# Performance work log

Measured on AMD Instinct MI355X. Metric: run time of the kernel, lower is better.

The kernel has to match this reference:

```python
import jax, jax.numpy as jnp
import numpy as np

N = 100000      # nodes
E = 1600000     # edges (avg degree 16)
DIN = 128
DH = 128
DOUT = 64
K = 2           # SGConv propagation steps
EPS = 1e-5      # BatchNorm eps


def setup_inputs() -> dict:
    key = jax.random.key(0)
    ks = jax.random.split(key, 12)
    x = jax.random.normal(ks[0], (N, DIN), dtype=jnp.float32)
    edge_index = jax.random.randint(ks[1], (2, E), 0, N, dtype=jnp.int32)
    def lin(k, fin, fout):
        k1, k2 = jax.random.split(k)
        s = 1.0 / np.sqrt(fin)
        W = jax.random.uniform(k1, (fin, fout), jnp.float32, -s, s)
        b = jax.random.uniform(k2, (fout,), jnp.float32, -s, s)
        return W, b
    W1, b1 = lin(ks[2], DIN, DH)
    W2, b2 = lin(ks[3], DH, DH)
    W3, b3 = lin(ks[4], DH, DOUT)
    g1 = jnp.ones((DH,), jnp.float32); be1 = jnp.zeros((DH,), jnp.float32)
    g2 = jnp.ones((DH,), jnp.float32); be2 = jnp.zeros((DH,), jnp.float32)
    return {"x": x, "edge_index": edge_index,
            "W1": W1, "b1": b1, "g1": g1, "be1": be1,
            "W2": W2, "b2": b2, "g2": g2, "be2": be2,
            "W3": W3, "b3": b3}


def _sgc_propagate(h, row, col, norm):
    # h: [N, d]; gather source nodes, scale per-edge, scatter-add to dest
    for _ in range(K):
        msg = norm[:, None] * h[row]                      # [E, d]
        h = jax.ops.segment_sum(msg, col, num_segments=N)  # [N, d]
    return h


def _batchnorm(h, gamma, beta):
    # training-mode BN over node axis, biased variance (torch semantics)
    mu = jnp.mean(h, axis=0)
    var = jnp.mean(jnp.square(h - mu), axis=0)
    return gamma * (h - mu) * jax.lax.rsqrt(var + EPS) + beta


def reference(x, edge_index, W1, b1, g1, be1, W2, b2, g2, be2, W3, b3):
    row, col = edge_index[0], edge_index[1]
    # symmetric degree normalization; degree counted on row (as in source)
    deg = jax.ops.segment_sum(jnp.ones((E,), x.dtype), row, num_segments=N)
    dis = jnp.where(deg > 0, 1.0 / jnp.sqrt(jnp.maximum(deg, 1.0)), 0.0)
    norm = dis[row] * dis[col]                             # [E]

    h = _sgc_propagate(x, row, col, norm)
    h = _batchnorm(h @ W1 + b1, g1, be1)   # dropout p=0.0 -> identity
    h = _sgc_propagate(h, row, col, norm)
    h = _batchnorm(h @ W2 + b2, g2, be2)
    return h @ W3 + b3                      # [N, DOUT]
```

## Files before the change

kernel.cpp:

```cpp
#include <hip/hip_runtime.h>
#include <hip/hip_fp16.h>


typedef _Float16 f16x8 __attribute__((ext_vector_type(8)));
typedef __attribute__((ext_vector_type(4))) float f32x4;

#define HR_RBITS 15
#define HR_RSIZE 32768
#define HR_NRANGE 4
#define HR_NCHUNK 96
#define HR_WPC (HR_NRANGE * HR_RSIZE / 2)

#define PA_NCHUNK 256
#define PB_SHIFT 8

static inline size_t align256(size_t x) { return (x + 255) & ~(size_t)255; }

__device__ inline unsigned int packh2(float a, float b) {
    return (unsigned int)__half_as_ushort(__float2half(a)) |
           ((unsigned int)__half_as_ushort(__float2half(b)) << 16);
}

__device__ inline void fmamix_lo(float& acc, unsigned int u, float w) {
    asm("v_fma_mix_f32 %0, %1, %2, %0 op_sel_hi:[1,0,0]"
        : "+v"(acc) : "v"(u), "v"(w));
}
__device__ inline void fmamix_hi(float& acc, unsigned int u, float w) {
    asm("v_fma_mix_f32 %0, %1, %2, %0 op_sel:[1,0,0] op_sel_hi:[1,0,0]"
        : "+v"(acc) : "v"(u), "v"(w));
}

__global__ void hist_row_kernel(const int* __restrict__ row, int E,
                                unsigned int* __restrict__ staging) {
    __shared__ unsigned int l32[HR_RSIZE / 2];
    int range = blockIdx.x % HR_NRANGE;
    int chunk = blockIdx.x / HR_NRANGE;
    for (int i = threadIdx.x; i < HR_RSIZE / 2; i += 256) l32[i] = 0;
    __syncthreads();
    int lo = range << HR_RBITS;
    int q4 = E >> 2;
    int ebeg = (int)(((long long)q4 * chunk / HR_NCHUNK) << 2);
    int eend = (int)(((long long)q4 * (chunk + 1) / HR_NCHUNK) << 2);
    for (int i = ebeg + threadIdx.x * 4; i + 3 < eend; i += 256 * 4) {
        int4 v = *(const int4*)(row + i);
        unsigned a;
        a = (unsigned)(v.x - lo); if (a < HR_RSIZE) atomicAdd(&l32[a >> 1], (a & 1) ? 0x10000u : 1u);
        a = (unsigned)(v.y - lo); if (a < HR_RSIZE) atomicAdd(&l32[a >> 1], (a & 1) ? 0x10000u : 1u);
        a = (unsigned)(v.z - lo); if (a < HR_RSIZE) atomicAdd(&l32[a >> 1], (a & 1) ? 0x10000u : 1u);
        a = (unsigned)(v.w - lo); if (a < HR_RSIZE) atomicAdd(&l32[a >> 1], (a & 1) ? 0x10000u : 1u);
    }
    if (chunk == HR_NCHUNK - 1) {
        for (int i = (E & ~3) + threadIdx.x; i < E; i += 256) {
            unsigned a = (unsigned)(row[i] - lo);
            if (a < HR_RSIZE) atomicAdd(&l32[a >> 1], (a & 1) ? 0x10000u : 1u);
        }
    }
    __syncthreads();
    unsigned int* dst = staging + (size_t)chunk * HR_WPC + (lo >> 1);
    for (int i = threadIdx.x; i < HR_RSIZE / 2; i += 256) dst[i] = l32[i];
}

__global__ void dis_kernel(const unsigned int* __restrict__ staging, float* __restrict__ dis, int n) {
    int i = blockIdx.x * blockDim.x + threadIdx.x;
    if (i < n) {
        int shift = (i & 1) * 16;
        int d = 0;
#pragma unroll 4
        for (int c = 0; c < HR_NCHUNK; ++c)
            d += (staging[(size_t)c * HR_WPC + (i >> 1)] >> shift) & 0xffff;
        dis[i] = d > 0 ? rsqrtf((float)d) : 0.f;
    }
}


__global__ void pa_hist_kernel(const int* __restrict__ col, int E,
                               int* __restrict__ chunkhist, int nbuck) {
    __shared__ int lh[512];
    int chunk = blockIdx.x;
    for (int i = threadIdx.x; i < nbuck; i += 256) lh[i] = 0;
    __syncthreads();
    int ebeg = (int)((long long)E * chunk / PA_NCHUNK);
    int eend = (int)((long long)E * (chunk + 1) / PA_NCHUNK);
    for (int i = ebeg + threadIdx.x; i < eend; i += 256)
        atomicAdd(&lh[col[i] >> PB_SHIFT], 1);
    __syncthreads();
    for (int i = threadIdx.x; i < nbuck; i += 256)
        chunkhist[i * PA_NCHUNK + chunk] = lh[i];
}

__global__ void pa_scan1_kernel(int* __restrict__ chunkhist, int* __restrict__ tot) {
    __shared__ int sh[PA_NCHUNK];
    int b = blockIdx.x, t = threadIdx.x;
    int* p = chunkhist + b * PA_NCHUNK;
    int v = p[t];
    sh[t] = v;
    __syncthreads();
    for (int off = 1; off < PA_NCHUNK; off <<= 1) {
        int tv = (t >= off) ? sh[t - off] : 0;
        __syncthreads();
        sh[t] += tv;
        __syncthreads();
    }
    p[t] = sh[t] - v;
    if (t == PA_NCHUNK - 1) tot[b] = sh[t];
}

__global__ void pa_scan2_kernel(const int* __restrict__ tot, int* __restrict__ bucketstart,
                                int nbuck) {
    __shared__ int sh[512];
    int t = threadIdx.x;
    int v = (t < nbuck) ? tot[t] : 0;
    sh[t] = v;
    __syncthreads();
    for (int off = 1; off < 512; off <<= 1) {
        int tv = (t >= off) ? sh[t - off] : 0;
        __syncthreads();
        sh[t] += tv;
        __syncthreads();
    }
    if (t < nbuck) bucketstart[t] = sh[t] - v;
    if (t == 511) bucketstart[nbuck] = sh[511];
}

__global__ void pa_scatter_kernel(const int* __restrict__ row, const int* __restrict__ col,
                                  int E, const int* __restrict__ chunkhist,
                                  const int* __restrict__ bucketstart,
                                  int2* __restrict__ part, int nbuck) {
    __shared__ int loff[512];
    int chunk = blockIdx.x;
    for (int i = threadIdx.x; i < nbuck; i += 256)
        loff[i] = chunkhist[i * PA_NCHUNK + chunk] + bucketstart[i];
    __syncthreads();
    int ebeg = (int)((long long)E * chunk / PA_NCHUNK);
    int eend = (int)((long long)E * (chunk + 1) / PA_NCHUNK);
    for (int i = ebeg + threadIdx.x; i < eend; i += 256) {
        int r = row[i], c = col[i];
        int pos = atomicAdd(&loff[c >> PB_SHIFT], 1);
        int2 v; v.x = r; v.y = c;
        part[pos] = v;
    }
}

__global__ void pb_kernel(const int2* __restrict__ part, const int* __restrict__ bucketstart,
                          const float* __restrict__ dis, int2* __restrict__ csr,
                          int* __restrict__ csr_ptr, int n) {
    __shared__ int lcnt[256], sh[256], loff[256];
    int b = blockIdx.x, t = threadIdx.x;
    int nlo = b << PB_SHIFT;
    int ebeg = bucketstart[b], eend = bucketstart[b + 1];
    lcnt[t] = 0;
    __syncthreads();
    for (int i = ebeg + t; i < eend; i += 256)
        atomicAdd(&lcnt[part[i].y - nlo], 1);
    __syncthreads();
    int v = lcnt[t];
    sh[t] = v;
    __syncthreads();
    for (int off = 1; off < 256; off <<= 1) {
        int tv = (t >= off) ? sh[t - off] : 0;
        __syncthreads();
        sh[t] += tv;
        __syncthreads();
    }
    int excl = sh[t] - v;
    loff[t] = excl;
    if (nlo + t <= n) csr_ptr[nlo + t] = ebeg + excl;
    __syncthreads();
    for (int i = ebeg + t; i < eend; i += 256) {
        int2 e = part[i];
        int c = e.y;
        int slot = atomicAdd(&loff[c - nlo], 1);
        int2 o;
        o.x = e.x;
        o.y = __float_as_int(dis[e.x] * dis[c]);
        csr[ebeg + slot] = o;
    }
}


__global__ void xcvt_kernel(const float* __restrict__ x, unsigned int* __restrict__ x16, int total4) {
    for (int i = blockIdx.x * blockDim.x + threadIdx.x; i < total4; i += gridDim.x * blockDim.x) {
        float4 f = ((const float4*)x)[i];
        x16[i * 2] = packh2(f.x, f.y);
        x16[i * 2 + 1] = packh2(f.z, f.w);
    }
}

__global__ void wcvt_kernel(const float* __restrict__ W1, const float* __restrict__ W2,
                            unsigned short* __restrict__ W1t, unsigned short* __restrict__ W2t) {
    int i = blockIdx.x * blockDim.x + threadIdx.x;
    if (i < 32768) {
        const float* W = (i < 16384) ? W1 : W2;
        unsigned short* T = (i < 16384) ? W1t : W2t;
        int j = i & 16383;
        int k = j >> 7, c = j & 127;
        T[c * 128 + k] = __half_as_ushort(__float2half(W[j]));
    }
}


template <bool AFF>
__global__ void spmm16_kernel(const int* __restrict__ csr_ptr, const int2* __restrict__ csr,
                              const unsigned short* __restrict__ h_in,
                              const float* __restrict__ scale, const float* __restrict__ shift,
                              unsigned short* __restrict__ h_out, int n) {
    int gw = __builtin_amdgcn_readfirstlane((blockIdx.x * blockDim.x + threadIdx.x) >> 6);
    int lane = threadIdx.x & 63;
    int sub = lane & 15;
    int grp = lane >> 4;
    if (gw >= n) return;
    uint4* outp = (uint4*)(h_out + (size_t)gw * 128) + sub;
    int beg = csr_ptr[gw];
    int end = csr_ptr[gw + 1];
    int cnt = end - beg;
    if (cnt == 0) {
        if (lane < 16) {
            uint4 z = {0u, 0u, 0u, 0u};
            *outp = z;
        }
        return;
    }
    const int2* base = csr + beg;
    const unsigned short* hb = h_in + sub * 8;
    float acc[8];
#pragma unroll
    for (int j = 0; j < 8; ++j) acc[j] = 0.f;
    float wsum = 0.f;
    for (int j0 = 0; j0 < cnt; j0 += 16) {
        int2 ent[4];
#pragma unroll
        for (int k = 0; k < 4; ++k) ent[k] = base[j0 + 4 * k + grp];
        uint4 u[4];
        float w[4];
#pragma unroll
        for (int k = 0; k < 4; ++k) {
            bool v = (j0 + 4 * k + grp) < cnt;
            int idx = v ? ent[k].x : 0;
            w[k] = v ? __int_as_float(ent[k].y) : 0.f;
            u[k] = *(const uint4*)(hb + (size_t)((unsigned)idx * 128u));
        }
#pragma unroll
        for (int k = 0; k < 4; ++k) {
            if (AFF) wsum += w[k];
            fmamix_lo(acc[0], u[k].x, w[k]);
            fmamix_hi(acc[1], u[k].x, w[k]);
            fmamix_lo(acc[2], u[k].y, w[k]);
            fmamix_hi(acc[3], u[k].y, w[k]);
            fmamix_lo(acc[4], u[k].z, w[k]);
            fmamix_hi(acc[5], u[k].z, w[k]);
            fmamix_lo(acc[6], u[k].w, w[k]);
            fmamix_hi(acc[7], u[k].w, w[k]);
        }
    }
#pragma unroll
    for (int j = 0; j < 8; ++j) {
        acc[j] += __shfl_xor(acc[j], 16, 64);
        acc[j] += __shfl_xor(acc[j], 32, 64);
    }
    if (AFF) {
        wsum += __shfl_xor(wsum, 16, 64);
        wsum += __shfl_xor(wsum, 32, 64);
        float4 s0 = ((const float4*)scale)[sub * 2];
        float4 s1 = ((const float4*)scale)[sub * 2 + 1];
        float4 h0 = ((const float4*)shift)[sub * 2];
        float4 h1 = ((const float4*)shift)[sub * 2 + 1];
        acc[0] = fmaf(h0.x, wsum, s0.x * acc[0]);
        acc[1] = fmaf(h0.y, wsum, s0.y * acc[1]);
        acc[2] = fmaf(h0.z, wsum, s0.z * acc[2]);
        acc[3] = fmaf(h0.w, wsum, s0.w * acc[3]);
        acc[4] = fmaf(h1.x, wsum, s1.x * acc[4]);
        acc[5] = fmaf(h1.y, wsum, s1.y * acc[5]);
        acc[6] = fmaf(h1.z, wsum, s1.z * acc[6]);
        acc[7] = fmaf(h1.w, wsum, s1.w * acc[7]);
    }
    if (lane < 16) {
        uint4 o;
        o.x = packh2(acc[0], acc[1]);
        o.y = packh2(acc[2], acc[3]);
        o.z = packh2(acc[4], acc[5]);
        o.w = packh2(acc[6], acc[7]);
        *outp = o;
    }
}


template <int NCT, bool OUTF32, bool STATS>
__launch_bounds__(256)
__global__ void gemm16_kernel(const unsigned short* __restrict__ X,
                              const unsigned short* __restrict__ Wt,
                              const float* __restrict__ bias, void* __restrict__ Y,
                              float* __restrict__ gsum, float* __restrict__ gsq, int n) {
    __shared__ __align__(16) char lds[NCT * 16 * 256];
    __shared__ float ssum[NCT * 16], ssq[NCT * 16];
    for (int i = threadIdx.x; i < NCT * 16 * 16; i += 256) {
        int col = i >> 4;
        int kbyte = (i & 15) << 4;
        *(uint4*)(lds + col * 256 + (kbyte ^ ((col & 7) << 4))) = ((const uint4*)Wt)[i];
    }
    if (STATS) {
        for (int i = threadIdx.x; i < NCT * 16; i += 256) {
            ssum[i] = 0.f;
            ssq[i] = 0.f;
        }
    }
    __syncthreads();

    int lane = threadIdx.x & 63;
    int wave = threadIdx.x >> 6;
    int cl = lane & 15, g = lane >> 4;

    f16x8 b[NCT][4];
#pragma unroll
    for (int ct = 0; ct < NCT; ++ct) {
        int col = ct * 16 + cl;
#pragma unroll
        for (int kc = 0; kc < 4; ++kc) {
            int kbyte = kc * 64 + g * 16;
            b[ct][kc] = *(const f16x8*)(lds + col * 256 + (kbyte ^ ((col & 7) << 4)));
        }
    }
    float bc[NCT];
#pragma unroll
    for (int ct = 0; ct < NCT; ++ct) bc[ct] = bias[ct * 16 + cl];

    for (int rb0 = blockIdx.x * 64; rb0 < n; rb0 += gridDim.x * 64) {
        int rb = rb0 + wave * 16;
        if (rb >= n) continue;
        int row = rb + cl;
        int rowc = row < n ? row : n - 1;
        const unsigned short* xr = X + (size_t)rowc * 128;
        f16x8 a[4];
#pragma unroll
        for (int kc = 0; kc < 4; ++kc) a[kc] = *(const f16x8*)(xr + kc * 32 + g * 8);
#pragma unroll
        for (int ct = 0; ct < NCT; ++ct) {
            f32x4 acc = {bc[ct], bc[ct], bc[ct], bc[ct]};
#pragma unroll
            for (int kc = 0; kc < 4; ++kc)
                acc = __builtin_amdgcn_mfma_f32_16x16x32_f16(a[kc], b[ct][kc], acc, 0, 0, 0);
            int colo = ct * 16 + cl;
            if (STATS) {
                float s = acc[0] + acc[1] + acc[2] + acc[3];
                float q = acc[0] * acc[0] + acc[1] * acc[1] + acc[2] * acc[2] + acc[3] * acc[3];
                s += __shfl_xor(s, 16, 64);
                s += __shfl_xor(s, 32, 64);
                q += __shfl_xor(q, 16, 64);
                q += __shfl_xor(q, 32, 64);
                if (g == 0) {
                    atomicAdd(&ssum[colo], s);
                    atomicAdd(&ssq[colo], q);
                }
            }
#pragma unroll
            for (int i = 0; i < 4; ++i) {
                int ro = rb + g * 4 + i;
                if (ro < n) {
                    if (OUTF32)
                        ((float*)Y)[(size_t)ro * (NCT * 16) + colo] = acc[i];
                    else
                        ((unsigned short*)Y)[(size_t)ro * 128 + colo] =
                            __half_as_ushort(__float2half(acc[i]));
                }
            }
        }
    }
    if (STATS) {
        __syncthreads();
        for (int i = threadIdx.x; i < NCT * 16; i += 256) {
            atomicAdd(&gsum[i], ssum[i]);
            atomicAdd(&gsq[i], ssq[i]);
        }
    }
}


__global__ void bn_final_kernel(const float* __restrict__ gsum, const float* __restrict__ gsq,
                                const float* __restrict__ gamma, const float* __restrict__ beta,
                                int n, float* __restrict__ scale, float* __restrict__ shift) {
    int c = threadIdx.x;
    if (c < 128) {
        float fn = (float)n;
        float mu = gsum[c] / fn;
        float var = gsq[c] / fn - mu * mu;
        float inv = rsqrtf(var + 1e-5f);
        float sc = gamma[c] * inv;
        scale[c] = sc;
        shift[c] = beta[c] - sc * mu;
    }
}

__global__ void fold_w3_kernel(const float* __restrict__ W3, const float* __restrict__ b3,
                               const float* __restrict__ scale, const float* __restrict__ shift,
                               unsigned short* __restrict__ W3t, float* __restrict__ b3f) {
    int c = threadIdx.x;
    if (c < 64) {
        float acc = b3[c];
        for (int k = 0; k < 128; ++k) {
            float w = W3[k * 64 + c];
            W3t[c * 128 + k] = __half_as_ushort(__float2half(scale[k] * w));
            acc += shift[k] * w;
        }
        b3f[c] = acc;
    }
}


extern "C" void kernel_launch(void* const* d_in, const int* in_sizes, int n_in,
                              void* d_out, int out_size, void* d_ws, size_t ws_size,
                              hipStream_t stream) {
    const float* x = (const float*)d_in[0];
    const int* edge = (const int*)d_in[1];
    const float* W1 = (const float*)d_in[2];
    const float* b1 = (const float*)d_in[3];
    const float* g1 = (const float*)d_in[4];
    const float* be1 = (const float*)d_in[5];
    const float* W2 = (const float*)d_in[6];
    const float* b2 = (const float*)d_in[7];
    const float* g2 = (const float*)d_in[8];
    const float* be2 = (const float*)d_in[9];
    const float* W3 = (const float*)d_in[10];
    const float* b3 = (const float*)d_in[11];
    float* out = (float*)d_out;

    const int N = in_sizes[0] / 128;
    const int E = in_sizes[1] / 2;
    const int* erow = edge;
    const int* ecol = edge + E;
    const int nbuck = (N + 255) >> PB_SHIFT;

    char* p = (char*)d_ws;
    size_t off = 0;
    auto carve = [&](size_t bytes) {
        void* r = p + off;
        off += align256(bytes);
        return r;
    };
    unsigned short* x16 = (unsigned short*)carve((size_t)N * 128 * 2);
    unsigned short* A16 = (unsigned short*)carve((size_t)N * 128 * 2);
    unsigned short* B16 = (unsigned short*)carve((size_t)N * 128 * 2);
    int2* part = (int2*)carve((size_t)E * 8);
    int2* csr = (int2*)carve((size_t)E * 8 + 256);
    int* csr_ptr = (int*)carve((size_t)(N + 1) * 4);
    int* chunkhist = (int*)carve((size_t)(nbuck + 1) * PA_NCHUNK * 4);
    int* bucketstart = (int*)carve((size_t)(nbuck + 1) * 4);
    int* tot = (int*)carve((size_t)(nbuck + 1) * 4);
    float* dis = (float*)carve((size_t)N * 4);
    float* gsum = (float*)carve(1024);
    float* gsq = (float*)(gsum + 128);
    float* scale1 = (float*)carve(512);
    float* shift1 = (float*)carve(512);
    float* scale2 = (float*)carve(512);
    float* shift2 = (float*)carve(512);
    unsigned short* W1t = (unsigned short*)carve(128 * 128 * 2);
    unsigned short* W2t = (unsigned short*)carve(128 * 128 * 2);
    unsigned short* W3t = (unsigned short*)carve(64 * 128 * 2);
    float* b3f = (float*)carve(256);
    unsigned int* staging = (unsigned int*)part;
    (void)ws_size;

    const int TB = 256;
    const int gN = (N + TB - 1) / TB;
    const int gSp = (N + 3) / 4;
    const int gGemm = (N + 63) / 64;
    const int gGemmS = 320;

    hist_row_kernel<<<HR_NRANGE * HR_NCHUNK, TB, 0, stream>>>(erow, E, staging);
    dis_kernel<<<gN, TB, 0, stream>>>(staging, dis, N);
    pa_hist_kernel<<<PA_NCHUNK, TB, 0, stream>>>(ecol, E, chunkhist, nbuck);
    pa_scan1_kernel<<<nbuck, PA_NCHUNK, 0, stream>>>(chunkhist, tot);
    pa_scan2_kernel<<<1, 512, 0, stream>>>(tot, bucketstart, nbuck);
    pa_scatter_kernel<<<PA_NCHUNK, TB, 0, stream>>>(erow, ecol, E, chunkhist, bucketstart, part, nbuck);
    pb_kernel<<<nbuck, TB, 0, stream>>>(part, bucketstart, dis, csr, csr_ptr, N);

    xcvt_kernel<<<2048, TB, 0, stream>>>(x, (unsigned int*)x16, N * 32);
    wcvt_kernel<<<128, TB, 0, stream>>>(W1, W2, W1t, W2t);

    spmm16_kernel<false><<<gSp, TB, 0, stream>>>(csr_ptr, csr, x16, nullptr, nullptr, A16, N);
    spmm16_kernel<false><<<gSp, TB, 0, stream>>>(csr_ptr, csr, A16, nullptr, nullptr, B16, N);

    hipMemsetAsync(gsum, 0, 1024, stream);
    gemm16_kernel<8, false, true><<<gGemmS, TB, 0, stream>>>(B16, W1t, b1, A16, gsum, gsq, N);
    bn_final_kernel<<<1, 128, 0, stream>>>(gsum, gsq, g1, be1, N, scale1, shift1);

    spmm16_kernel<true><<<gSp, TB, 0, stream>>>(csr_ptr, csr, A16, scale1, shift1, B16, N);
    spmm16_kernel<false><<<gSp, TB, 0, stream>>>(csr_ptr, csr, B16, nullptr, nullptr, A16, N);

    hipMemsetAsync(gsum, 0, 1024, stream);
    gemm16_kernel<8, false, true><<<gGemmS, TB, 0, stream>>>(A16, W2t, b2, B16, gsum, gsq, N);
    bn_final_kernel<<<1, 128, 0, stream>>>(gsum, gsq, g2, be2, N, scale2, shift2);

    fold_w3_kernel<<<1, 64, 0, stream>>>(W3, b3, scale2, shift2, W3t, b3f);
    gemm16_kernel<4, true, false><<<gGemm, TB, 0, stream>>>(B16, W3t, b3f, out, nullptr, nullptr, N);
}
```

Before: 399.3 us.

## Pack row-degree histogram into 8-bit counters and compress partition entries to 32 bits

The row-degree histogram now packs four 8-bit counters per 32-bit LDS word. This covers 65536 nodes per block with 2 ranges and 128 chunks, so fewer redundant passes over the edge array are needed. The partition buffer stores each edge as a single int (row<<8 | local col), which halves its write and read traffic in the scatter and bucket-sort stages. The feature GEMMs also switch from a fixed 320-block grid to one block per 64 rows. The 8-bit counters overflow if a node gets more than 255 edges within one chunk, and the packing assumes row indices fit in 24 bits.

```diff
diff --git a/kernel.cpp b/kernel.cpp
--- a/kernel.cpp
+++ b/kernel.cpp
@@ -5,11 +5,11 @@
 typedef _Float16 f16x8 __attribute__((ext_vector_type(8)));
 typedef __attribute__((ext_vector_type(4))) float f32x4;
 
-#define HR_RBITS 15
-#define HR_RSIZE 32768
-#define HR_NRANGE 4
-#define HR_NCHUNK 96
-#define HR_WPC (HR_NRANGE * HR_RSIZE / 2)
+#define HR_RBITS 16
+#define HR_RSIZE 65536
+#define HR_NRANGE 2
+#define HR_NCHUNK 128
+#define HR_WPC (HR_NRANGE * HR_RSIZE / 4)
 
 #define PA_NCHUNK 256
 #define PB_SHIFT 8
@@ -32,10 +32,10 @@
 
 __global__ void hist_row_kernel(const int* __restrict__ row, int E,
                                 unsigned int* __restrict__ staging) {
-    __shared__ unsigned int l32[HR_RSIZE / 2];
+    __shared__ unsigned int l32[HR_RSIZE / 4];
     int range = blockIdx.x % HR_NRANGE;
     int chunk = blockIdx.x / HR_NRANGE;
-    for (int i = threadIdx.x; i < HR_RSIZE / 2; i += 256) l32[i] = 0;
+    for (int i = threadIdx.x; i < HR_RSIZE / 4; i += 256) l32[i] = 0;
     __syncthreads();
     int lo = range << HR_RBITS;
     int q4 = E >> 2;
@@ -44,30 +44,30 @@
     for (int i = ebeg + threadIdx.x * 4; i + 3 < eend; i += 256 * 4) {
         int4 v = *(const int4*)(row + i);
         unsigned a;
-        a = (unsigned)(v.x - lo); if (a < HR_RSIZE) atomicAdd(&l32[a >> 1], (a & 1) ? 0x10000u : 1u);
-        a = (unsigned)(v.y - lo); if (a < HR_RSIZE) atomicAdd(&l32[a >> 1], (a & 1) ? 0x10000u : 1u);
-        a = (unsigned)(v.z - lo); if (a < HR_RSIZE) atomicAdd(&l32[a >> 1], (a & 1) ? 0x10000u : 1u);
-        a = (unsigned)(v.w - lo); if (a < HR_RSIZE) atomicAdd(&l32[a >> 1], (a & 1) ? 0x10000u : 1u);
+        a = (unsigned)(v.x - lo); if (a < HR_RSIZE) atomicAdd(&l32[a >> 2], 1u << ((a & 3) * 8));
+        a = (unsigned)(v.y - lo); if (a < HR_RSIZE) atomicAdd(&l32[a >> 2], 1u << ((a & 3) * 8));
+        a = (unsigned)(v.z - lo); if (a < HR_RSIZE) atomicAdd(&l32[a >> 2], 1u << ((a & 3) * 8));
+        a = (unsigned)(v.w - lo); if (a < HR_RSIZE) atomicAdd(&l32[a >> 2], 1u << ((a & 3) * 8));
     }
     if (chunk == HR_NCHUNK - 1) {
         for (int i = (E & ~3) + threadIdx.x; i < E; i += 256) {
             unsigned a = (unsigned)(row[i] - lo);
-            if (a < HR_RSIZE) atomicAdd(&l32[a >> 1], (a & 1) ? 0x10000u : 1u);
-        }
-    }
-    __syncthreads();
-    unsigned int* dst = staging + (size_t)chunk * HR_WPC + (lo >> 1);
-    for (int i = threadIdx.x; i < HR_RSIZE / 2; i += 256) dst[i] = l32[i];
+            if (a < HR_RSIZE) atomicAdd(&l32[a >> 2], 1u << ((a & 3) * 8));
+        }
+    }
+    __syncthreads();
+    unsigned int* dst = staging + (size_t)chunk * HR_WPC + (lo >> 2);
+    for (int i = threadIdx.x; i < HR_RSIZE / 4; i += 256) dst[i] = l32[i];
 }
 
 __global__ void dis_kernel(const unsigned int* __restrict__ staging, float* __restrict__ dis, int n) {
     int i = blockIdx.x * blockDim.x + threadIdx.x;
     if (i < n) {
-        int shift = (i & 1) * 16;
+        int shift = (i & 3) * 8;
         int d = 0;
 #pragma unroll 4
         for (int c = 0; c < HR_NCHUNK; ++c)
-            d += (staging[(size_t)c * HR_WPC + (i >> 1)] >> shift) & 0xffff;
+            d += (staging[(size_t)c * HR_WPC + (i >> 2)] >> shift) & 0xff;
         dis[i] = d > 0 ? rsqrtf((float)d) : 0.f;
     }
 }
@@ -125,7 +125,7 @@
 __global__ void pa_scatter_kernel(const int* __restrict__ row, const int* __restrict__ col,
                                   int E, const int* __restrict__ chunkhist,
                                   const int* __restrict__ bucketstart,
-                                  int2* __restrict__ part, int nbuck) {
+                                  int* __restrict__ part, int nbuck) {
     __shared__ int loff[512];
     int chunk = blockIdx.x;
     for (int i = threadIdx.x; i < nbuck; i += 256)
@@ -136,12 +136,11 @@
     for (int i = ebeg + threadIdx.x; i < eend; i += 256) {
         int r = row[i], c = col[i];
         int pos = atomicAdd(&loff[c >> PB_SHIFT], 1);
-        int2 v; v.x = r; v.y = c;
-        part[pos] = v;
-    }
-}
-
-__global__ void pb_kernel(const int2* __restrict__ part, const int* __restrict__ bucketstart,
+        part[pos] = (r << 8) | (c & 255);
+    }
+}
+
+__global__ void pb_kernel(const int* __restrict__ part, const int* __restrict__ bucketstart,
                           const float* __restrict__ dis, int2* __restrict__ csr,
                           int* __restrict__ csr_ptr, int n) {
     __shared__ int lcnt[256], sh[256], loff[256];
@@ -151,7 +150,7 @@
     lcnt[t] = 0;
     __syncthreads();
     for (int i = ebeg + t; i < eend; i += 256)
-        atomicAdd(&lcnt[part[i].y - nlo], 1);
+        atomicAdd(&lcnt[part[i] & 255], 1);
     __syncthreads();
     int v = lcnt[t];
     sh[t] = v;
@@ -167,12 +166,13 @@
     if (nlo + t <= n) csr_ptr[nlo + t] = ebeg + excl;
     __syncthreads();
     for (int i = ebeg + t; i < eend; i += 256) {
-        int2 e = part[i];
-        int c = e.y;
-        int slot = atomicAdd(&loff[c - nlo], 1);
+        int e = part[i];
+        int cl8 = e & 255;
+        int r = (int)((unsigned)e >> 8);
+        int slot = atomicAdd(&loff[cl8], 1);
         int2 o;
-        o.x = e.x;
-        o.y = __float_as_int(dis[e.x] * dis[c]);
+        o.x = r;
+        o.y = __float_as_int(dis[r] * dis[nlo + cl8]);
         csr[ebeg + slot] = o;
     }
 }
@@ -438,7 +438,7 @@
     unsigned short* x16 = (unsigned short*)carve((size_t)N * 128 * 2);
     unsigned short* A16 = (unsigned short*)carve((size_t)N * 128 * 2);
     unsigned short* B16 = (unsigned short*)carve((size_t)N * 128 * 2);
-    int2* part = (int2*)carve((size_t)E * 8);
+    int* part = (int*)carve((size_t)E * 4);
     int2* csr = (int2*)carve((size_t)E * 8 + 256);
     int* csr_ptr = (int*)carve((size_t)(N + 1) * 4);
     int* chunkhist = (int*)carve((size_t)(nbuck + 1) * PA_NCHUNK * 4);
@@ -462,7 +462,6 @@
     const int gN = (N + TB - 1) / TB;
     const int gSp = (N + 3) / 4;
     const int gGemm = (N + 63) / 64;
-    const int gGemmS = 320;
 
     hist_row_kernel<<<HR_NRANGE * HR_NCHUNK, TB, 0, stream>>>(erow, E, staging);
     dis_kernel<<<gN, TB, 0, stream>>>(staging, dis, N);
@@ -479,14 +478,14 @@
     spmm16_kernel<false><<<gSp, TB, 0, stream>>>(csr_ptr, csr, A16, nullptr, nullptr, B16, N);
 
     hipMemsetAsync(gsum, 0, 1024, stream);
-    gemm16_kernel<8, false, true><<<gGemmS, TB, 0, stream>>>(B16, W1t, b1, A16, gsum, gsq, N);
+    gemm16_kernel<8, false, true><<<gGemm, TB, 0, stream>>>(B16, W1t, b1, A16, gsum, gsq, N);
     bn_final_kernel<<<1, 128, 0, stream>>>(gsum, gsq, g1, be1, N, scale1, shift1);
 
     spmm16_kernel<true><<<gSp, TB, 0, stream>>>(csr_ptr, csr, A16, scale1, shift1, B16, N);
     spmm16_kernel<false><<<gSp, TB, 0, stream>>>(csr_ptr, csr, B16, nullptr, nullptr, A16, N);
 
     hipMemsetAsync(gsum, 0, 1024, stream);
-    gemm16_kernel<8, false, true><<<gGemmS, TB, 0, stream>>>(A16, W2t, b2, B16, gsum, gsq, N);
+    gemm16_kernel<8, false, true><<<gGemm, TB, 0, stream>>>(A16, W2t, b2, B16, gsum, gsq, N);
     bn_final_kernel<<<1, 128, 0, stream>>>(gsum, gsq, g2, be2, N, scale2, shift2);
 
     fold_w3_kernel<<<1, 64, 0, stream>>>(W3, b3, scale2, shift2, W3t, b3f);
```

New measurement: 435.4 us. 1.09x slower.
